# Kernel tuning notes

Hardware: AMD Instinct MI355X
Metric: run time of the kernel (lower is better)

Reference implementation:

```python
import jax, jax.numpy as jnp
import numpy as np

S = 14
STEP = 1.0 / S
LAMBDA_COORD = 7.0
LAMBDA_NOOBJ = 0.2
LAMBDA_CLS = 1.5
EPS = 1e-06


def _xywh_to_xyxy(box):
    # box: [N, S, S, 2, 4]; grid offset i = column (axis 2), j = row (axis 1)
    gx = jnp.arange(S, dtype=box.dtype)[None, None, :, None]
    gy = jnp.arange(S, dtype=box.dtype)[None, :, None, None]
    x = (box[..., 0] + gx) * STEP
    y = (box[..., 1] + gy) * STEP
    w = box[..., 2]
    h = box[..., 3]
    return jnp.stack([x - w / 2, y - h / 2, x + w / 2, y + h / 2], axis=-1)


def _iou(b1, b2):
    # b1, b2: [..., 4] xyxy, elementwise IoU
    x1 = jnp.maximum(b1[..., 0], b2[..., 0])
    y1 = jnp.maximum(b1[..., 1], b2[..., 1])
    x2 = jnp.minimum(b1[..., 2], b2[..., 2])
    y2 = jnp.minimum(b1[..., 3], b2[..., 3])
    inter = jnp.maximum(x2 - x1, 0.0) * jnp.maximum(y2 - y1, 0.0)
    area1 = (b1[..., 2] - b1[..., 0]) * (b1[..., 3] - b1[..., 1])
    area2 = (b2[..., 2] - b2[..., 0]) * (b2[..., 3] - b2[..., 1])
    union = area1 + area2 - inter + EPS
    return inter / union


def _ciou_loss(b1, b2):
    # b1 = pred xyxy, b2 = target xyxy (both already include grid offsets)
    iou = _iou(b1, b2)
    cx1 = (b1[..., 0] + b1[..., 2]) / 2
    cy1 = (b1[..., 1] + b1[..., 3]) / 2
    cx2 = (b2[..., 0] + b2[..., 2]) / 2
    cy2 = (b2[..., 1] + b2[..., 3]) / 2
    center_dist = (cx1 - cx2) ** 2 + (cy1 - cy2) ** 2
    x_c1 = jnp.minimum(b1[..., 0], b2[..., 0])
    y_c1 = jnp.minimum(b1[..., 1], b2[..., 1])
    x_c2 = jnp.maximum(b1[..., 2], b2[..., 2])
    y_c2 = jnp.maximum(b1[..., 3], b2[..., 3])
    outer_diag = (x_c2 - x_c1) ** 2 + (y_c2 - y_c1) ** 2 + EPS
    w1 = jnp.maximum(b1[..., 2] - b1[..., 0], EPS)
    h1 = jnp.maximum(b1[..., 3] - b1[..., 1], EPS)
    w2 = jnp.maximum(b2[..., 2] - b2[..., 0], EPS)
    h2 = jnp.maximum(b2[..., 3] - b2[..., 1], EPS)
    v = 4.0 / (jnp.pi ** 2) * (jnp.arctan(w2 / h2) - jnp.arctan(w1 / h1)) ** 2
    alpha = v / (1.0 - iou + v + EPS)
    ciou = iou - center_dist / outer_diag - alpha * v
    scale = jnp.maximum(2.0 - w2 * h2, 1.0)
    return (1.0 - ciou) * scale


def setup_inputs() -> dict:
    key = jax.random.key(0)
    k1, k2, k3 = jax.random.split(key, 3)
    N = 4096
    pred = jax.random.uniform(k1, (N, S, S, 30), dtype=jnp.float32)
    target = jax.random.uniform(k2, (N, S, S, 30), dtype=jnp.float32)
    # both anchor boxes of a cell share the same objectness, as in YOLOv1 encoding.
    obj_cell = jax.random.uniform(k3, (N, S, S)) < 0.1
    conf0 = jnp.where(obj_cell, jnp.maximum(target[..., 4], 0.5), 0.0)
    conf1 = jnp.where(obj_cell, jnp.maximum(target[..., 9], 0.5), 0.0)
    target = target.at[..., 4].set(conf0).at[..., 9].set(conf1)
    return {"pred": pred, "target": target}


def reference(pred, target):
    N = pred.shape[0]
    tb = target[..., :10].reshape(N, S, S, 2, 5)
    pb = pred[..., :10].reshape(N, S, S, 2, 5)
    tcls = target[..., 10:]
    pcls = pred[..., 10:]

    obj = tb[..., 4] > 0            # [N,S,S,2]
    sig = obj[..., 1]               # [N,S,S]

    b1 = _xywh_to_xyxy(pb[..., :4])  # pred
    b2 = _xywh_to_xyxy(tb[..., :4])  # target

    # responsible box per object cell: argmax IoU over the 2 predictors
    iou = _iou(b1, b2)               # [N,S,S,2]
    resp = jnp.argmax(iou, axis=-1)  # [N,S,S]
    suppress = sig[..., None] & (jnp.arange(2) == (1 - resp)[..., None])
    obj_m = obj & ~suppress
    noobj_m = ~obj_m

    dconf = (pb[..., 4] - tb[..., 4]) ** 2
    obj_loss = jnp.sum(jnp.where(obj_m, dconf, 0.0))
    noobj_loss = jnp.sum(jnp.where(noobj_m, dconf, 0.0))

    ciou = _ciou_loss(b1, b2)        # [N,S,S,2]
    bbox_loss = jnp.sum(jnp.where(sig[..., None] & obj_m, ciou, 0.0))

    p = jnp.clip(pcls, 1e-07, 1.0 - 1e-07)
    bce = -(tcls * jnp.log(p) + (1.0 - tcls) * jnp.log1p(-p))
    class_loss = jnp.sum(jnp.where(sig[..., None], bce, 0.0)) * LAMBDA_CLS

    loss = obj_loss + LAMBDA_NOOBJ * noobj_loss + LAMBDA_COORD * bbox_loss + class_loss
    return loss / N
```

## Files before the change

### kernel.cpp

```cpp
#include <hip/hip_runtime.h>
#include <stdint.h>

#define S 14
#define NBATCH 4096
#define TOTAL (NBATCH * S * S)
#define TPB   256
#define TILE_CELLS 64
#define NT    2
#define CPB   (TILE_CELLS * NT)
#define GRID  (TOTAL / CPB)
#define TILE_TB (TILE_CELLS * 120)
#define NCHUNKS 18

constexpr float STEP_C       = 1.0f / 14.0f;
constexpr float EPS_C        = 1e-6f;
constexpr float LAMBDA_NOOBJ = 0.2f;
constexpr float LAMBDA_COORD = 7.0f;
constexpr float LAMBDA_CLS   = 1.5f;
constexpr float INV_N        = 1.0f / (float)NBATCH;
constexpr float C_V          = 0.40528473456935109f;

__device__ __forceinline__ void gload16(const char* gsrc, char* lds_dst) {
    __builtin_amdgcn_global_load_lds(
        (const __attribute__((address_space(1))) void*)gsrc,
        (__attribute__((address_space(3))) void*)lds_dst, 16, 0, 0);
}
__device__ __forceinline__ void gload4(const char* gsrc, char* lds_dst) {
    __builtin_amdgcn_global_load_lds(
        (const __attribute__((address_space(1))) void*)gsrc,
        (__attribute__((address_space(3))) void*)lds_dst, 4, 0, 0);
}

__device__ __forceinline__ void stage_tile(const char* gp, const char* gt,
                                           int t, char* buf, int wid, int lane) {
    const size_t toff = (size_t)t * TILE_TB;
    for (int c = wid; c < NCHUNKS; c += 4) {
        int tensor = (c >= 9) ? 1 : 0;
        int kk = c - tensor * 9;
        const char* sbase = (tensor ? gt : gp) + toff;
        char* dbase = buf + tensor * TILE_TB;
        if (kk < 7) gload16(sbase + kk * 1024 + lane * 16, dbase + kk * 1024);
        else        gload4 (sbase + 7168 + (kk - 7) * 256 + lane * 4,
                            dbase + 7168 + (kk - 7) * 256);
    }
}

__global__ __launch_bounds__(TPB) void yolo_loss_kernel(
    const float* __restrict__ pred, const float* __restrict__ target,
    float* __restrict__ partial) {
    __shared__ __align__(16) char sbuf[2][2 * TILE_TB];
    __shared__ int   slist[2][64];
    __shared__ float ws[4];

    const int tid  = threadIdx.x;
    const int lane = tid & 63;
    const int wid  = tid >> 6;

    const char* gp = reinterpret_cast<const char*>(pred)   + (size_t)blockIdx.x * NT * TILE_TB;
    const char* gt = reinterpret_cast<const char*>(target) + (size_t)blockIdx.x * NT * TILE_TB;

    float contrib = 0.0f;

    stage_tile(gp, gt, 0, sbuf[0], wid, lane);

    #pragma unroll
    for (int t = 0; t < NT; ++t) {
        if (t + 1 < NT) stage_tile(gp, gt, t + 1, sbuf[t + 1], wid, lane);

        if (t + 1 < NT) {
            if (wid < 2) asm volatile("s_waitcnt vmcnt(5)" ::: "memory");
            else         asm volatile("s_waitcnt vmcnt(4)" ::: "memory");
        } else {
            asm volatile("s_waitcnt vmcnt(0)" ::: "memory");
        }
        __builtin_amdgcn_sched_barrier(0);
        __builtin_amdgcn_s_barrier();
        __builtin_amdgcn_sched_barrier(0);

        const float* sp = reinterpret_cast<const float*>(sbuf[t]);
        const float* st = reinterpret_cast<const float*>(sbuf[t] + TILE_TB);

        if (wid == (t & 1)) {
            const int rbase = lane * 30;

            float t4 = st[rbase + 4], t9 = st[rbase + 9];
            float p4 = sp[rbase + 4], p9 = sp[rbase + 9];
            float d0 = p4 - t4;
            float d1 = p9 - t9;
            bool  sig = t4 > 0.0f;
            contrib += LAMBDA_NOOBJ * (d0 * d0 + d1 * d1);

            unsigned long long mask = __ballot(sig);
            int nsig = __popcll(mask);

            if (sig) {
                int rank = __popcll(mask & ((1ull << lane) - 1ull));
                slist[t][rank] = lane;

                int cell = blockIdx.x * CPB + t * TILE_CELLS + lane;
                int j = cell % S;
                int i = (cell / S) % S;
                float gx = (float)j, gy = (float)i;

                float p0 = sp[rbase + 0], p1 = sp[rbase + 1], p2 = sp[rbase + 2], p3 = sp[rbase + 3];
                float p5 = sp[rbase + 5], p6 = sp[rbase + 6], p7 = sp[rbase + 7], p8 = sp[rbase + 8];
                float t0 = st[rbase + 0], t1 = st[rbase + 1], t2 = st[rbase + 2], t3 = st[rbase + 3];
                float t5 = st[rbase + 5], t6 = st[rbase + 6], t7 = st[rbase + 7], t8 = st[rbase + 8];

                float P0x = (p0 + gx) * STEP_C, P0y = (p1 + gy) * STEP_C;
                float P1x = (p5 + gx) * STEP_C, P1y = (p6 + gy) * STEP_C;
                float T0x = (t0 + gx) * STEP_C, T0y = (t1 + gy) * STEP_C;
                float T1x = (t5 + gx) * STEP_C, T1y = (t6 + gy) * STEP_C;

                float a0x0 = P0x - p2 * 0.5f, a0y0 = P0y - p3 * 0.5f;
                float a0x1 = P0x + p2 * 0.5f, a0y1 = P0y + p3 * 0.5f;
                float a1x0 = P1x - p7 * 0.5f, a1y0 = P1y - p8 * 0.5f;
                float a1x1 = P1x + p7 * 0.5f, a1y1 = P1y + p8 * 0.5f;
                float b0x0 = T0x - t2 * 0.5f, b0y0 = T0y - t3 * 0.5f;
                float b0x1 = T0x + t2 * 0.5f, b0y1 = T0y + t3 * 0.5f;
                float b1x0 = T1x - t7 * 0.5f, b1y0 = T1y - t8 * 0.5f;
                float b1x1 = T1x + t7 * 0.5f, b1y1 = T1y + t8 * 0.5f;

                float i0x1 = fmaxf(a0x0, b0x0), i0y1 = fmaxf(a0y0, b0y0);
                float i0x2 = fminf(a0x1, b0x1), i0y2 = fminf(a0y1, b0y1);
                float inter0 = fmaxf(i0x2 - i0x1, 0.0f) * fmaxf(i0y2 - i0y1, 0.0f);
                float ar0a = (a0x1 - a0x0) * (a0y1 - a0y0);
                float ar0b = (b0x1 - b0x0) * (b0y1 - b0y0);
                float iou0 = inter0 / (ar0a + ar0b - inter0 + EPS_C);

                float i1x1 = fmaxf(a1x0, b1x0), i1y1 = fmaxf(a1y0, b1y0);
                float i1x2 = fminf(a1x1, b1x1), i1y2 = fminf(a1y1, b1y1);
                float inter1 = fmaxf(i1x2 - i1x1, 0.0f) * fmaxf(i1y2 - i1y1, 0.0f);
                float ar1a = (a1x1 - a1x0) * (a1y1 - a1y0);
                float ar1b = (b1x1 - b1x0) * (b1y1 - b1y0);
                float iou1 = inter1 / (ar1a + ar1b - inter1 + EPS_C);

                bool r1 = iou1 > iou0;

                float dr = r1 ? d1 : d0;
                contrib += (1.0f - LAMBDA_NOOBJ) * dr * dr;

                float ax0 = r1 ? a1x0 : a0x0, ay0 = r1 ? a1y0 : a0y0;
                float ax1 = r1 ? a1x1 : a0x1, ay1 = r1 ? a1y1 : a0y1;
                float bx0 = r1 ? b1x0 : b0x0, by0 = r1 ? b1y0 : b0y0;
                float bx1 = r1 ? b1x1 : b0x1, by1 = r1 ? b1y1 : b0y1;
                float iou = r1 ? iou1 : iou0;

                float cx1 = (ax0 + ax1) * 0.5f, cy1 = (ay0 + ay1) * 0.5f;
                float cx2 = (bx0 + bx1) * 0.5f, cy2 = (by0 + by1) * 0.5f;
                float cd = (cx1 - cx2) * (cx1 - cx2) + (cy1 - cy2) * (cy1 - cy2);
                float xc1 = fminf(ax0, bx0), yc1 = fminf(ay0, by0);
                float xc2 = fmaxf(ax1, bx1), yc2 = fmaxf(ay1, by1);
                float od = (xc2 - xc1) * (xc2 - xc1) + (yc2 - yc1) * (yc2 - yc1) + EPS_C;
                float w1 = fmaxf(ax1 - ax0, EPS_C), h1 = fmaxf(ay1 - ay0, EPS_C);
                float w2 = fmaxf(bx1 - bx0, EPS_C), h2 = fmaxf(by1 - by0, EPS_C);
                float dd = atanf(w2 / h2) - atanf(w1 / h1);
                float vv = C_V * dd * dd;
                float alpha = vv / (1.0f - iou + vv + EPS_C);
                float ciou = iou - cd / od - alpha * vv;
                float scale = fmaxf(2.0f - w2 * h2, 1.0f);
                contrib += LAMBDA_COORD * (1.0f - ciou) * scale;
            }

            asm volatile("s_waitcnt lgkmcnt(0)" ::: "memory");
            __builtin_amdgcn_sched_barrier(0);

            float s = 0.0f;
            int nitems = nsig * 20;
            for (int q = lane; q < nitems; q += 64) {
                int ciq = q / 20;
                int cls = q - ciq * 20;
                int r2  = slist[t][ciq] * 30 + 10 + cls;
                float pc = sp[r2];
                float tc = st[r2];
                pc = fminf(fmaxf(pc, 1e-7f), 1.0f - 1e-7f);
                s += tc * __logf(pc) + (1.0f - tc) * __logf(1.0f - pc);
            }
            contrib -= LAMBDA_CLS * s;
        }
    }

    float r = contrib;
    #pragma unroll
    for (int off = 32; off > 0; off >>= 1) r += __shfl_down(r, off);
    if (lane == 0) ws[wid] = r;
    __syncthreads();
    if (tid == 0)
        partial[blockIdx.x] = ws[0] + ws[1] + ws[2] + ws[3];
}

__global__ __launch_bounds__(1024) void yolo_reduce_kernel(
    const float* __restrict__ partial, float* __restrict__ out) {
    const int tid  = threadIdx.x;
    const int lane = tid & 63;
    const int wid  = tid >> 6;

    float s = 0.0f;
    for (int i = tid; i < GRID; i += 1024) s += partial[i];

    #pragma unroll
    for (int off = 32; off > 0; off >>= 1) s += __shfl_down(s, off);

    __shared__ float ws[16];
    if (lane == 0) ws[wid] = s;
    __syncthreads();
    if (tid == 0) {
        float sum = 0.0f;
        #pragma unroll
        for (int w = 0; w < 16; ++w) sum += ws[w];
        out[0] = sum * INV_N;
    }
}

extern "C" void kernel_launch(void* const* d_in, const int* in_sizes, int n_in,
                              void* d_out, int out_size, void* d_ws, size_t ws_size,
                              hipStream_t stream) {
    const float* pred   = (const float*)d_in[0];
    const float* target = (const float*)d_in[1];
    float* out     = (float*)d_out;
    float* partial = (float*)d_ws;

    hipLaunchKernelGGL(yolo_loss_kernel, dim3(GRID), dim3(TPB), 0, stream,
                       pred, target, partial);
    hipLaunchKernelGGL(yolo_reduce_kernel, dim3(1), dim3(1024), 0, stream,
                       partial, out);
}
```

Baseline: 39.41 us.

## Give each wave its own double-buffered multi-tile pipeline without block barriers

Restructures the kernel so each 64-lane wave independently streams 8 tiles of 32 cells through its own double-buffered LDS region, replacing the 256-thread block where loads were shared across waves but only one wave computed per tile under a block barrier. This removes s_barrier synchronisation and lets all waves compute concurrently, and it writes one partial per wave. In exchange, half the lanes sit idle during the per-cell stage (32 cells per 64-lane wave), and deeper per-wave vmcnt pipelining adds LDS pressure per block.

After: 44.23 us. 12.2% more time.

```diff
diff --git a/kernel.cpp b/kernel.cpp
--- a/kernel.cpp
+++ b/kernel.cpp
@@ -4,13 +4,15 @@
 #define S 14
 #define NBATCH 4096
 #define TOTAL (NBATCH * S * S)
-#define TPB   256
-#define TILE_CELLS 64
-#define NT    2
-#define CPB   (TILE_CELLS * NT)
+#define TPB   128
+#define TILE_CELLS 32
+#define NT    8
+#define CPW   (TILE_CELLS * NT)
+#define CPB   (CPW * 2)
 #define GRID  (TOTAL / CPB)
+#define NPART (GRID * 2)
 #define TILE_TB (TILE_CELLS * 120)
-#define NCHUNKS 18
+#define TILE_BYTES (2 * TILE_TB)
 
 constexpr float STEP_C       = 1.0f / 14.0f;
 constexpr float EPS_C        = 1e-6f;
@@ -31,146 +33,142 @@
         (__attribute__((address_space(3))) void*)lds_dst, 4, 0, 0);
 }
 
-__device__ __forceinline__ void stage_tile(const char* gp, const char* gt,
-                                           int t, char* buf, int wid, int lane) {
-    const size_t toff = (size_t)t * TILE_TB;
-    for (int c = wid; c < NCHUNKS; c += 4) {
-        int tensor = (c >= 9) ? 1 : 0;
-        int kk = c - tensor * 9;
-        const char* sbase = (tensor ? gt : gp) + toff;
-        char* dbase = buf + tensor * TILE_TB;
-        if (kk < 7) gload16(sbase + kk * 1024 + lane * 16, dbase + kk * 1024);
-        else        gload4 (sbase + 7168 + (kk - 7) * 256 + lane * 4,
-                            dbase + 7168 + (kk - 7) * 256);
-    }
+__device__ __forceinline__ void stage_tensor(const char* src, char* dst, int lane) {
+    #pragma unroll
+    for (int c = 0; c < 3; ++c) gload16(src + c * 1024 + lane * 16, dst + c * 1024);
+    #pragma unroll
+    for (int c = 0; c < 3; ++c) gload4(src + 3072 + c * 256 + lane * 4, dst + 3072 + c * 256);
 }
 
 __global__ __launch_bounds__(TPB) void yolo_loss_kernel(
     const float* __restrict__ pred, const float* __restrict__ target,
     float* __restrict__ partial) {
-    __shared__ __align__(16) char sbuf[2][2 * TILE_TB];
-    __shared__ int   slist[2][64];
-    __shared__ float ws[4];
-
-    const int tid  = threadIdx.x;
-    const int lane = tid & 63;
-    const int wid  = tid >> 6;
-
-    const char* gp = reinterpret_cast<const char*>(pred)   + (size_t)blockIdx.x * NT * TILE_TB;
-    const char* gt = reinterpret_cast<const char*>(target) + (size_t)blockIdx.x * NT * TILE_TB;
+    __shared__ __align__(16) char sbuf[2][2][TILE_BYTES];
+    __shared__ int slist[2][2][TILE_CELLS];
+
+    const int lane = threadIdx.x & 63;
+    const int wid  = threadIdx.x >> 6;
+
+    const char* gp = reinterpret_cast<const char*>(pred)
+                   + ((size_t)blockIdx.x * CPB + (size_t)wid * CPW) * 120;
+    const char* gt = reinterpret_cast<const char*>(target)
+                   + ((size_t)blockIdx.x * CPB + (size_t)wid * CPW) * 120;
 
     float contrib = 0.0f;
 
-    stage_tile(gp, gt, 0, sbuf[0], wid, lane);
-
-    #pragma unroll
+    stage_tensor(gp, sbuf[wid][0], lane);
+    stage_tensor(gt, sbuf[wid][0] + TILE_TB, lane);
+
     for (int t = 0; t < NT; ++t) {
-        if (t + 1 < NT) stage_tile(gp, gt, t + 1, sbuf[t + 1], wid, lane);
-
         if (t + 1 < NT) {
-            if (wid < 2) asm volatile("s_waitcnt vmcnt(5)" ::: "memory");
-            else         asm volatile("s_waitcnt vmcnt(4)" ::: "memory");
-        } else {
-            asm volatile("s_waitcnt vmcnt(0)" ::: "memory");
-        }
+            const size_t off = (size_t)(t + 1) * TILE_TB;
+            char* nb = sbuf[wid][(t + 1) & 1];
+            stage_tensor(gp + off, nb, lane);
+            stage_tensor(gt + off, nb + TILE_TB, lane);
+        }
+
+        if (t + 1 < NT) asm volatile("s_waitcnt vmcnt(12)" ::: "memory");
+        else            asm volatile("s_waitcnt vmcnt(0)"  ::: "memory");
         __builtin_amdgcn_sched_barrier(0);
-        __builtin_amdgcn_s_barrier();
-        __builtin_amdgcn_sched_barrier(0);
-
-        const float* sp = reinterpret_cast<const float*>(sbuf[t]);
-        const float* st = reinterpret_cast<const float*>(sbuf[t] + TILE_TB);
-
-        if (wid == (t & 1)) {
+
+        const float* sp = reinterpret_cast<const float*>(sbuf[wid][t & 1]);
+        const float* st = reinterpret_cast<const float*>(sbuf[wid][t & 1] + TILE_TB);
+
+        bool sig = false;
+        float d0 = 0.0f, d1 = 0.0f;
+        if (lane < TILE_CELLS) {
             const int rbase = lane * 30;
-
             float t4 = st[rbase + 4], t9 = st[rbase + 9];
             float p4 = sp[rbase + 4], p9 = sp[rbase + 9];
-            float d0 = p4 - t4;
-            float d1 = p9 - t9;
-            bool  sig = t4 > 0.0f;
+            d0 = p4 - t4;
+            d1 = p9 - t9;
+            sig = t4 > 0.0f;
             contrib += LAMBDA_NOOBJ * (d0 * d0 + d1 * d1);
-
-            unsigned long long mask = __ballot(sig);
-            int nsig = __popcll(mask);
-
-            if (sig) {
-                int rank = __popcll(mask & ((1ull << lane) - 1ull));
-                slist[t][rank] = lane;
-
-                int cell = blockIdx.x * CPB + t * TILE_CELLS + lane;
-                int j = cell % S;
-                int i = (cell / S) % S;
-                float gx = (float)j, gy = (float)i;
-
-                float p0 = sp[rbase + 0], p1 = sp[rbase + 1], p2 = sp[rbase + 2], p3 = sp[rbase + 3];
-                float p5 = sp[rbase + 5], p6 = sp[rbase + 6], p7 = sp[rbase + 7], p8 = sp[rbase + 8];
-                float t0 = st[rbase + 0], t1 = st[rbase + 1], t2 = st[rbase + 2], t3 = st[rbase + 3];
-                float t5 = st[rbase + 5], t6 = st[rbase + 6], t7 = st[rbase + 7], t8 = st[rbase + 8];
-
-                float P0x = (p0 + gx) * STEP_C, P0y = (p1 + gy) * STEP_C;
-                float P1x = (p5 + gx) * STEP_C, P1y = (p6 + gy) * STEP_C;
-                float T0x = (t0 + gx) * STEP_C, T0y = (t1 + gy) * STEP_C;
-                float T1x = (t5 + gx) * STEP_C, T1y = (t6 + gy) * STEP_C;
-
-                float a0x0 = P0x - p2 * 0.5f, a0y0 = P0y - p3 * 0.5f;
-                float a0x1 = P0x + p2 * 0.5f, a0y1 = P0y + p3 * 0.5f;
-                float a1x0 = P1x - p7 * 0.5f, a1y0 = P1y - p8 * 0.5f;
-                float a1x1 = P1x + p7 * 0.5f, a1y1 = P1y + p8 * 0.5f;
-                float b0x0 = T0x - t2 * 0.5f, b0y0 = T0y - t3 * 0.5f;
-                float b0x1 = T0x + t2 * 0.5f, b0y1 = T0y + t3 * 0.5f;
-                float b1x0 = T1x - t7 * 0.5f, b1y0 = T1y - t8 * 0.5f;
-                float b1x1 = T1x + t7 * 0.5f, b1y1 = T1y + t8 * 0.5f;
-
-                float i0x1 = fmaxf(a0x0, b0x0), i0y1 = fmaxf(a0y0, b0y0);
-                float i0x2 = fminf(a0x1, b0x1), i0y2 = fminf(a0y1, b0y1);
-                float inter0 = fmaxf(i0x2 - i0x1, 0.0f) * fmaxf(i0y2 - i0y1, 0.0f);
-                float ar0a = (a0x1 - a0x0) * (a0y1 - a0y0);
-                float ar0b = (b0x1 - b0x0) * (b0y1 - b0y0);
-                float iou0 = inter0 / (ar0a + ar0b - inter0 + EPS_C);
-
-                float i1x1 = fmaxf(a1x0, b1x0), i1y1 = fmaxf(a1y0, b1y0);
-                float i1x2 = fminf(a1x1, b1x1), i1y2 = fminf(a1y1, b1y1);
-                float inter1 = fmaxf(i1x2 - i1x1, 0.0f) * fmaxf(i1y2 - i1y1, 0.0f);
-                float ar1a = (a1x1 - a1x0) * (a1y1 - a1y0);
-                float ar1b = (b1x1 - b1x0) * (b1y1 - b1y0);
-                float iou1 = inter1 / (ar1a + ar1b - inter1 + EPS_C);
-
-                bool r1 = iou1 > iou0;
-
-                float dr = r1 ? d1 : d0;
-                contrib += (1.0f - LAMBDA_NOOBJ) * dr * dr;
-
-                float ax0 = r1 ? a1x0 : a0x0, ay0 = r1 ? a1y0 : a0y0;
-                float ax1 = r1 ? a1x1 : a0x1, ay1 = r1 ? a1y1 : a0y1;
-                float bx0 = r1 ? b1x0 : b0x0, by0 = r1 ? b1y0 : b0y0;
-                float bx1 = r1 ? b1x1 : b0x1, by1 = r1 ? b1y1 : b0y1;
-                float iou = r1 ? iou1 : iou0;
-
-                float cx1 = (ax0 + ax1) * 0.5f, cy1 = (ay0 + ay1) * 0.5f;
-                float cx2 = (bx0 + bx1) * 0.5f, cy2 = (by0 + by1) * 0.5f;
-                float cd = (cx1 - cx2) * (cx1 - cx2) + (cy1 - cy2) * (cy1 - cy2);
-                float xc1 = fminf(ax0, bx0), yc1 = fminf(ay0, by0);
-                float xc2 = fmaxf(ax1, bx1), yc2 = fmaxf(ay1, by1);
-                float od = (xc2 - xc1) * (xc2 - xc1) + (yc2 - yc1) * (yc2 - yc1) + EPS_C;
-                float w1 = fmaxf(ax1 - ax0, EPS_C), h1 = fmaxf(ay1 - ay0, EPS_C);
-                float w2 = fmaxf(bx1 - bx0, EPS_C), h2 = fmaxf(by1 - by0, EPS_C);
-                float dd = atanf(w2 / h2) - atanf(w1 / h1);
-                float vv = C_V * dd * dd;
-                float alpha = vv / (1.0f - iou + vv + EPS_C);
-                float ciou = iou - cd / od - alpha * vv;
-                float scale = fmaxf(2.0f - w2 * h2, 1.0f);
-                contrib += LAMBDA_COORD * (1.0f - ciou) * scale;
-            }
-
-            asm volatile("s_waitcnt lgkmcnt(0)" ::: "memory");
-            __builtin_amdgcn_sched_barrier(0);
-
+        }
+
+        unsigned long long mask = __ballot(sig);
+        int nsig = __popcll(mask);
+
+        if (sig) {
+            int rank = __popcll(mask & ((1ull << lane) - 1ull));
+            slist[wid][t & 1][rank] = lane;
+
+            const int rbase = lane * 30;
+            int cell = blockIdx.x * CPB + wid * CPW + t * TILE_CELLS + lane;
+            int j = cell % S;
+            int i = (cell / S) % S;
+            float gx = (float)j, gy = (float)i;
+
+            float p0 = sp[rbase + 0], p1 = sp[rbase + 1], p2 = sp[rbase + 2], p3 = sp[rbase + 3];
+            float p5 = sp[rbase + 5], p6 = sp[rbase + 6], p7 = sp[rbase + 7], p8 = sp[rbase + 8];
+            float t0 = st[rbase + 0], t1 = st[rbase + 1], t2 = st[rbase + 2], t3 = st[rbase + 3];
+            float t5 = st[rbase + 5], t6 = st[rbase + 6], t7 = st[rbase + 7], t8 = st[rbase + 8];
+
+            float P0x = (p0 + gx) * STEP_C, P0y = (p1 + gy) * STEP_C;
+            float P1x = (p5 + gx) * STEP_C, P1y = (p6 + gy) * STEP_C;
+            float T0x = (t0 + gx) * STEP_C, T0y = (t1 + gy) * STEP_C;
+            float T1x = (t5 + gx) * STEP_C, T1y = (t6 + gy) * STEP_C;
+
+            float a0x0 = P0x - p2 * 0.5f, a0y0 = P0y - p3 * 0.5f;
+            float a0x1 = P0x + p2 * 0.5f, a0y1 = P0y + p3 * 0.5f;
+            float a1x0 = P1x - p7 * 0.5f, a1y0 = P1y - p8 * 0.5f;
+            float a1x1 = P1x + p7 * 0.5f, a1y1 = P1y + p8 * 0.5f;
+            float b0x0 = T0x - t2 * 0.5f, b0y0 = T0y - t3 * 0.5f;
+            float b0x1 = T0x + t2 * 0.5f, b0y1 = T0y + t3 * 0.5f;
+            float b1x0 = T1x - t7 * 0.5f, b1y0 = T1y - t8 * 0.5f;
+            float b1x1 = T1x + t7 * 0.5f, b1y1 = T1y + t8 * 0.5f;
+
+            float i0x1 = fmaxf(a0x0, b0x0), i0y1 = fmaxf(a0y0, b0y0);
+            float i0x2 = fminf(a0x1, b0x1), i0y2 = fminf(a0y1, b0y1);
+            float inter0 = fmaxf(i0x2 - i0x1, 0.0f) * fmaxf(i0y2 - i0y1, 0.0f);
+            float ar0a = (a0x1 - a0x0) * (a0y1 - a0y0);
+            float ar0b = (b0x1 - b0x0) * (b0y1 - b0y0);
+            float iou0 = inter0 / (ar0a + ar0b - inter0 + EPS_C);
+
+            float i1x1 = fmaxf(a1x0, b1x0), i1y1 = fmaxf(a1y0, b1y0);
+            float i1x2 = fminf(a1x1, b1x1), i1y2 = fminf(a1y1, b1y1);
+            float inter1 = fmaxf(i1x2 - i1x1, 0.0f) * fmaxf(i1y2 - i1y1, 0.0f);
+            float ar1a = (a1x1 - a1x0) * (a1y1 - a1y0);
+            float ar1b = (b1x1 - b1x0) * (b1y1 - b1y0);
+            float iou1 = inter1 / (ar1a + ar1b - inter1 + EPS_C);
+
+            bool r1 = iou1 > iou0;
+
+            float dr = r1 ? d1 : d0;
+            contrib += (1.0f - LAMBDA_NOOBJ) * dr * dr;
+
+            float ax0 = r1 ? a1x0 : a0x0, ay0 = r1 ? a1y0 : a0y0;
+            float ax1 = r1 ? a1x1 : a0x1, ay1 = r1 ? a1y1 : a0y1;
+            float bx0 = r1 ? b1x0 : b0x0, by0 = r1 ? b1y0 : b0y0;
+            float bx1 = r1 ? b1x1 : b0x1, by1 = r1 ? b1y1 : b0y1;
+            float iou = r1 ? iou1 : iou0;
+
+            float cx1 = (ax0 + ax1) * 0.5f, cy1 = (ay0 + ay1) * 0.5f;
+            float cx2 = (bx0 + bx1) * 0.5f, cy2 = (by0 + by1) * 0.5f;
+            float cd = (cx1 - cx2) * (cx1 - cx2) + (cy1 - cy2) * (cy1 - cy2);
+            float xc1 = fminf(ax0, bx0), yc1 = fminf(ay0, by0);
+            float xc2 = fmaxf(ax1, bx1), yc2 = fmaxf(ay1, by1);
+            float od = (xc2 - xc1) * (xc2 - xc1) + (yc2 - yc1) * (yc2 - yc1) + EPS_C;
+            float w1 = fmaxf(ax1 - ax0, EPS_C), h1 = fmaxf(ay1 - ay0, EPS_C);
+            float w2 = fmaxf(bx1 - bx0, EPS_C), h2 = fmaxf(by1 - by0, EPS_C);
+            float dd = atanf(w2 / h2) - atanf(w1 / h1);
+            float vv = C_V * dd * dd;
+            float alpha = vv / (1.0f - iou + vv + EPS_C);
+            float ciou = iou - cd / od - alpha * vv;
+            float scale = fmaxf(2.0f - w2 * h2, 1.0f);
+            contrib += LAMBDA_COORD * (1.0f - ciou) * scale;
+        }
+
+        asm volatile("s_waitcnt lgkmcnt(0)" ::: "memory");
+        __builtin_amdgcn_sched_barrier(0);
+
+        {
             float s = 0.0f;
             int nitems = nsig * 20;
             for (int q = lane; q < nitems; q += 64) {
                 int ciq = q / 20;
                 int cls = q - ciq * 20;
-                int r2  = slist[t][ciq] * 30 + 10 + cls;
+                int r2  = slist[wid][t & 1][ciq] * 30 + 10 + cls;
                 float pc = sp[r2];
                 float tc = st[r2];
                 pc = fminf(fmaxf(pc, 1e-7f), 1.0f - 1e-7f);
@@ -178,15 +176,16 @@
             }
             contrib -= LAMBDA_CLS * s;
         }
+
+        asm volatile("s_waitcnt lgkmcnt(0)" ::: "memory");
+        __builtin_amdgcn_sched_barrier(0);
     }
 
     float r = contrib;
     #pragma unroll
     for (int off = 32; off > 0; off >>= 1) r += __shfl_down(r, off);
-    if (lane == 0) ws[wid] = r;
-    __syncthreads();
-    if (tid == 0)
-        partial[blockIdx.x] = ws[0] + ws[1] + ws[2] + ws[3];
+    if (lane == 0)
+        partial[blockIdx.x * 2 + wid] = r;
 }
 
 __global__ __launch_bounds__(1024) void yolo_reduce_kernel(
@@ -196,7 +195,7 @@
     const int wid  = tid >> 6;
 
     float s = 0.0f;
-    for (int i = tid; i < GRID; i += 1024) s += partial[i];
+    for (int i = tid; i < NPART; i += 1024) s += partial[i];
 
     #pragma unroll
     for (int off = 32; off > 0; off >>= 1) s += __shfl_down(s, off);
```
